# Optimization experiments

Measured on AMD Instinct MI355X. Metric: run time of the kernel, lower is better.

The kernel has to match this reference:

```python
import jax, jax.numpy as jnp
import numpy as np

NUM_HEADS = 16
EMB = 1024
HEAD = 64
SEQ = 2048
BATCH = 4


def setup_inputs() -> dict:
    key = jax.random.key(0)
    ks = jax.random.split(key, 6)
    s = EMB ** -0.5
    x = jax.random.normal(ks[0], (BATCH, SEQ, EMB), dtype=jnp.float32)
    # per-head projection weights stacked: [H, E, D] (Linear(emb, head, bias=False) per head)
    Wq = jax.random.normal(ks[1], (NUM_HEADS, EMB, HEAD), dtype=jnp.float32) * s
    Wk = jax.random.normal(ks[2], (NUM_HEADS, EMB, HEAD), dtype=jnp.float32) * s
    Wv = jax.random.normal(ks[3], (NUM_HEADS, EMB, HEAD), dtype=jnp.float32) * s
    # output projection Linear(head*num_heads, emb): weight [E, H*D], bias [E]
    Wo = jax.random.normal(ks[4], (EMB, NUM_HEADS * HEAD), dtype=jnp.float32) * ((NUM_HEADS * HEAD) ** -0.5)
    bo = jax.random.normal(ks[5], (EMB,), dtype=jnp.float32) * 0.01
    return {"x": x, "Wq": Wq, "Wk": Wk, "Wv": Wv, "Wo": Wo, "bo": bo}


def reference(x, Wq, Wk, Wv, Wo, bo):
    B, S, E = x.shape
    scale = HEAD ** -0.5
    # batched per-head projections: [B, H, S, D]
    q = jnp.einsum('bse,hed->bhsd', x, Wq)
    k = jnp.einsum('bse,hed->bhsd', x, Wk)
    v = jnp.einsum('bse,hed->bhsd', x, Wv)
    scores = jnp.einsum('bhqd,bhkd->bhqk', q, k) * scale
    causal = jnp.tril(jnp.ones((S, S), dtype=bool))
    scores = jnp.where(causal, scores, jnp.finfo(scores.dtype).min)
    attn = jax.nn.softmax(scores, axis=-1)  # dropout disabled (eval/deterministic)
    ctx = jnp.einsum('bhqk,bhkd->bhqd', attn, v)
    # concat heads along last dim (head-major order, matching torch.cat)
    concat = ctx.transpose(0, 2, 1, 3).reshape(B, S, NUM_HEADS * HEAD)
    out = concat @ Wo.T + bo
    return out
```

## Files before the change

kernel.cpp:

```cpp
#include <hip/hip_runtime.h>

#define NHEADS 16
#define EMB 1024
#define HDIM 64
#define SEQ 2048
#define BATCH 4

typedef unsigned short u16;
typedef __attribute__((ext_vector_type(8))) __bf16 bf16x8;
typedef __attribute__((ext_vector_type(4))) float f32x4;

#if __has_builtin(__builtin_amdgcn_exp2f)
#define EXP2(x) __builtin_amdgcn_exp2f(x)
#else
#define EXP2(x) __expf((x)*0.69314718056f)
#endif
#define CL2E 0.18033688011112042f

#define BARRIER() __builtin_amdgcn_s_barrier()
#define SB0() __builtin_amdgcn_sched_barrier(0)
#define PRIO1() __builtin_amdgcn_s_setprio(1)
#define PRIO0() __builtin_amdgcn_s_setprio(0)
#define VMCNT(n) asm volatile("s_waitcnt vmcnt(" #n ")" ::: "memory")
#define LGKM0() asm volatile("s_waitcnt lgkmcnt(0)" ::: "memory")

__device__ __forceinline__ u16 f2bf(float f) {
  union { float f; unsigned u; } v; v.f = f;
  unsigned r = v.u + 0x7fffu + ((v.u >> 16) & 1u);
  return (u16)(r >> 16);
}
__device__ __forceinline__ unsigned pk2bf(float a, float b) {
  union { __bf16 h[2]; unsigned u; } x;
  x.h[0] = (__bf16)a; x.h[1] = (__bf16)b; return x.u;
}
__device__ __forceinline__ void gl16(const void* g, void* l) {
  __builtin_amdgcn_global_load_lds(
      (const __attribute__((address_space(1))) unsigned*)g,
      (__attribute__((address_space(3))) unsigned*)l, 16, 0, 0);
}
__device__ __forceinline__ unsigned PKLO(unsigned a, unsigned b) {
  return __builtin_amdgcn_perm(a, b, 0x01000504u);
}
__device__ __forceinline__ unsigned PKHI(unsigned a, unsigned b) {
  return __builtin_amdgcn_perm(a, b, 0x03020706u);
}

__global__ __launch_bounds__(256) void k_prep(const float* __restrict__ x,
                                              const float* __restrict__ Wo,
                                              const float* __restrict__ Wq,
                                              const float* __restrict__ Wk,
                                              const float* __restrict__ Wv,
                                              u16* __restrict__ Xb,
                                              u16* __restrict__ Wob,
                                              u16* __restrict__ Wt) {
  __shared__ u16 sT[64][65];
  const int bid = blockIdx.x;
  const int t = threadIdx.x;
  if (bid < 8192) {
    int i = bid * 256 + t;
    f32x4 v = *(const f32x4*)(x + (size_t)i * 4);
    uint2 o;
    o.x = (unsigned)f2bf(v[0]) | ((unsigned)f2bf(v[1]) << 16);
    o.y = (unsigned)f2bf(v[2]) | ((unsigned)f2bf(v[3]) << 16);
    *(uint2*)(Xb + (size_t)i * 4) = o;
  } else if (bid < 9216) {
    int i = (bid - 8192) * 256 + t;
    f32x4 v = *(const f32x4*)(Wo + (size_t)i * 4);
    uint2 o;
    o.x = (unsigned)f2bf(v[0]) | ((unsigned)f2bf(v[1]) << 16);
    o.y = (unsigned)f2bf(v[2]) | ((unsigned)f2bf(v[3]) << 16);
    *(uint2*)(Wob + (size_t)i * 4) = o;
  } else {
    int pb = bid - 9216;
    const int mh = pb % 48;
    const int e0 = (pb / 48) * 64;
    const int mtx = mh >> 4, h = mh & 15;
    const float* W = (mtx == 0 ? Wq : (mtx == 1 ? Wk : Wv)) + (size_t)h * EMB * HDIM;
    {
      int e = t >> 2, d0 = (t & 3) * 16;
#pragma unroll
      for (int jj = 0; jj < 4; jj++) {
        f32x4 v = *(const f32x4*)(W + (size_t)(e0 + e) * HDIM + d0 + jj * 4);
#pragma unroll
        for (int kk = 0; kk < 4; kk++) sT[e][d0 + jj * 4 + kk] = f2bf(v[kk]);
      }
    }
    __syncthreads();
    {
      int d = t >> 2, eb = (t & 3) * 16;
#pragma unroll
      for (int j = 0; j < 16; j++)
        Wt[(size_t)(mh * 64 + d) * EMB + e0 + eb + j] = sT[eb + j][d];
    }
  }
}

__global__ __launch_bounds__(256) void k_gemm_qkv(const u16* __restrict__ Xb,
                                                  const u16* __restrict__ Wt,
                                                  u16* __restrict__ Q,
                                                  u16* __restrict__ K,
                                                  u16* __restrict__ V) {
  const int bid = blockIdx.x;
  const int l = (bid & 7) * 192 + (bid >> 3);
  const int mt = l % 64, nt = l / 64;
  const int m0 = mt * 128, n0 = nt * 128;
  const int t = threadIdx.x;
  const int wave = t >> 6, lane = t & 63, lr = lane & 15, lg = lane >> 4;
  const int wr = (wave >> 1) * 64, wc = (wave & 1) * 64;

  __shared__ __align__(16) char sA[128 * 128];
  __shared__ __align__(16) char sB[128 * 128];

  const f32x4 fz = {0.f, 0.f, 0.f, 0.f};
  f32x4 acc[4][4];
#pragma unroll
  for (int i = 0; i < 4; i++)
#pragma unroll
    for (int j = 0; j < 4; j++) acc[i][j] = fz;

  for (int k0 = 0; k0 < EMB; k0 += 64) {
#pragma unroll
    for (int i = 0; i < 4; i++) {
      int rb = wave * 32 + i * 8;
      int row = rb + (lane >> 3);
      int gc = (lane & 7) ^ (row & 7);
      gl16(Xb + (size_t)(m0 + row) * EMB + k0 + gc * 8, sA + rb * 128);
      gl16(Wt + (size_t)(n0 + row) * EMB + k0 + gc * 8, sB + rb * 128);
    }
    __syncthreads();
    bf16x8 af[4][2], bfr[4][2];
#pragma unroll
    for (int mf = 0; mf < 4; mf++)
#pragma unroll
      for (int kf = 0; kf < 2; kf++) {
        int row = wr + mf * 16 + lr;
        af[mf][kf] = *(const bf16x8*)(sA + row * 128 + ((kf * 64 + lg * 16) ^ ((row & 7) << 4)));
      }
#pragma unroll
    for (int nf = 0; nf < 4; nf++)
#pragma unroll
      for (int kf = 0; kf < 2; kf++) {
        int row = wc + nf * 16 + lr;
        bfr[nf][kf] = *(const bf16x8*)(sB + row * 128 + ((kf * 64 + lg * 16) ^ ((row & 7) << 4)));
      }
#pragma unroll
    for (int kf = 0; kf < 2; kf++)
#pragma unroll
      for (int mf = 0; mf < 4; mf++)
#pragma unroll
        for (int nf = 0; nf < 4; nf++)
          acc[mf][nf] = __builtin_amdgcn_mfma_f32_16x16x32_bf16(af[mf][kf], bfr[nf][kf], acc[mf][nf], 0, 0, 0);
    __syncthreads();
  }

  const int b = m0 >> 11;
  const int s0 = m0 & 2047;
#pragma unroll
  for (int mf = 0; mf < 4; mf++)
#pragma unroll
    for (int nf = 0; nf < 4; nf++)
#pragma unroll
      for (int r = 0; r < 4; r++) {
        int row = wr + mf * 16 + lg * 4 + r;
        int n = n0 + wc + nf * 16 + lr;
        int mtx = n >> 10, h = (n >> 6) & 15, d = n & 63;
        u16* dst = (mtx == 0 ? Q : (mtx == 1 ? K : V));
        dst[((size_t)(b * NHEADS + h) * SEQ + s0 + row) * HDIM + d] = f2bf(acc[mf][nf][r]);
      }
}

__global__ __launch_bounds__(256, 3) void k_attn(const u16* __restrict__ Q,
                                                 const u16* __restrict__ K,
                                                 const u16* __restrict__ V,
                                                 u16* __restrict__ Cc) {
  const int bh = blockIdx.x;
  const int qt = 15 - (int)blockIdx.y;
  const int b = bh >> 4, h = bh & 15;
  const int t = threadIdx.x;
  const int wq = t >> 6, lane = t & 63, lr = lane & 15, lg = lane >> 4;
  const size_t base = (size_t)bh * SEQ * HDIM;

  __shared__ __align__(16) char sK[2][64 * 128];
  __shared__ __align__(16) char sV[2][64 * 128];
  __shared__ __align__(16) char sP[128 * 128];

  const int kvb = (t & 15) * 4, db = (t >> 4) * 4;
  uint2 v0, v1, v2, v3;
  auto VLOAD = [&](int k0) {
    const u16* vp = V + base + (size_t)(k0 + kvb) * HDIM + db;
    v0 = *(const uint2*)(vp);
    v1 = *(const uint2*)(vp + HDIM);
    v2 = *(const uint2*)(vp + 2 * HDIM);
    v3 = *(const uint2*)(vp + 3 * HDIM);
  };
  auto VWRITE = [&](char* sv) {
    uint2 w0 = {PKLO(v0.x, v1.x), PKLO(v2.x, v3.x)};
    uint2 w1 = {PKHI(v0.x, v1.x), PKHI(v2.x, v3.x)};
    uint2 w2 = {PKLO(v0.y, v1.y), PKLO(v2.y, v3.y)};
    uint2 w3 = {PKHI(v0.y, v1.y), PKHI(v2.y, v3.y)};
    *(uint2*)(sv + (db + 0) * 128 + ((kvb * 2) ^ (((db + 0) & 7) << 4))) = w0;
    *(uint2*)(sv + (db + 1) * 128 + ((kvb * 2) ^ (((db + 1) & 7) << 4))) = w1;
    *(uint2*)(sv + (db + 2) * 128 + ((kvb * 2) ^ (((db + 2) & 7) << 4))) = w2;
    *(uint2*)(sv + (db + 3) * 128 + ((kvb * 2) ^ (((db + 3) & 7) << 4))) = w3;
  };
  auto KSTAGE = [&](char* sk, int k0) {
#pragma unroll
    for (int i = 0; i < 2; i++) {
      int rb = wq * 16 + i * 8;
      int row = rb + (lane >> 3);
      int gc = (lane & 7) ^ (row & 7);
      gl16(K + base + (size_t)(k0 + row) * HDIM + gc * 8, sk + rb * 128);
    }
  };

#pragma unroll
  for (int i = 0; i < 4; i++) {
    int rb = wq * 32 + i * 8;
    int row = rb + (lane >> 3);
    int gc = (lane & 7) ^ (row & 7);
    gl16(Q + base + (size_t)(qt * 128 + row) * HDIM + gc * 8, sP + rb * 128);
  }
  KSTAGE(sK[0], 0);
  VLOAD(0);
  VMCNT(0);
  VWRITE(sV[0]);
  __syncthreads();

  bf16x8 qf[2][2];
#pragma unroll
  for (int q2 = 0; q2 < 2; q2++)
#pragma unroll
    for (int kf = 0; kf < 2; kf++) {
      int row = wq * 32 + q2 * 16 + lr;
      qf[q2][kf] = *(const bf16x8*)(sP + row * 128 + ((kf * 64 + lg * 16) ^ ((row & 7) << 4)));
    }

  const f32x4 fz = {0.f, 0.f, 0.f, 0.f};
  f32x4 ot[4][2];
#pragma unroll
  for (int df = 0; df < 4; df++)
#pragma unroll
    for (int q2 = 0; q2 < 2; q2++) ot[df][q2] = fz;
  float l_[2] = {0.f, 0.f};
  const float nmc = -64.f * CL2E;

  const int nsteps = 2 * qt + 2;
  for (int step = 0; step < nsteps; step++) {
    const int k0 = step * 64;
    const int cur = step & 1, nxt = cur ^ 1;
    const bool pf = (step + 1 < nsteps);
    if (pf) {
      KSTAGE(sK[nxt], k0 + 64);
      VLOAD(k0 + 64);
    }

    f32x4 st[4][2];
#pragma unroll
    for (int kvf = 0; kvf < 4; kvf++)
#pragma unroll
      for (int q2 = 0; q2 < 2; q2++) st[kvf][q2] = fz;
#pragma unroll
    for (int kf = 0; kf < 2; kf++) {
      bf16x8 kfr[4];
#pragma unroll
      for (int kvf = 0; kvf < 4; kvf++) {
        int row = kvf * 16 + lr;
        kfr[kvf] = *(const bf16x8*)(sK[cur] + row * 128 + ((kf * 64 + lg * 16) ^ ((row & 7) << 4)));
      }
      PRIO1();
#pragma unroll
      for (int kvf = 0; kvf < 4; kvf++)
#pragma unroll
        for (int q2 = 0; q2 < 2; q2++)
          st[kvf][q2] = __builtin_amdgcn_mfma_f32_16x16x32_bf16(kfr[kvf], qf[q2][kf], st[kvf][q2], 0, 0, 0);
      PRIO0();
    }

    const bool diag = (k0 >= qt * 128);
#pragma unroll
    for (int q2 = 0; q2 < 2; q2++) {
      if (diag) {
        const int qg = qt * 128 + wq * 32 + q2 * 16 + lr;
#pragma unroll
        for (int kvf = 0; kvf < 4; kvf++)
#pragma unroll
          for (int r = 0; r < 4; r++)
            if (k0 + kvf * 16 + 4 * lg + r > qg) st[kvf][q2][r] = -3e38f;
      }
      const int prow = wq * 32 + q2 * 16 + lr;
      float rs = 0.f;
#pragma unroll
      for (int kvf = 0; kvf < 4; kvf++) {
        float p0 = EXP2(fmaf(st[kvf][q2][0], CL2E, nmc));
        float p1 = EXP2(fmaf(st[kvf][q2][1], CL2E, nmc));
        float p2 = EXP2(fmaf(st[kvf][q2][2], CL2E, nmc));
        float p3 = EXP2(fmaf(st[kvf][q2][3], CL2E, nmc));
        rs += (p0 + p1) + (p2 + p3);
        uint2 w;
        w.x = pk2bf(p0, p1);
        w.y = pk2bf(p2, p3);
        *(uint2*)(sP + prow * 128 + ((kvf * 32 + lg * 8) ^ ((prow & 7) << 4))) = w;
      }
      l_[q2] += rs;
    }

#pragma unroll
    for (int kf = 0; kf < 2; kf++) {
      bf16x8 pfg[2], vf[4];
#pragma unroll
      for (int q2 = 0; q2 < 2; q2++) {
        int row = wq * 32 + q2 * 16 + lr;
        pfg[q2] = *(const bf16x8*)(sP + row * 128 + ((kf * 64 + lg * 16) ^ ((row & 7) << 4)));
      }
#pragma unroll
      for (int df = 0; df < 4; df++) {
        int row = df * 16 + lr;
        vf[df] = *(const bf16x8*)(sV[cur] + row * 128 + ((kf * 64 + lg * 16) ^ ((row & 7) << 4)));
      }
      PRIO1();
#pragma unroll
      for (int df = 0; df < 4; df++)
#pragma unroll
        for (int q2 = 0; q2 < 2; q2++)
          ot[df][q2] = __builtin_amdgcn_mfma_f32_16x16x32_bf16(vf[df], pfg[q2], ot[df][q2], 0, 0, 0);
      PRIO0();
    }

    if (pf) {
      VMCNT(0);
      VWRITE(sV[nxt]);
      LGKM0();
      BARRIER();
    }
  }

#pragma unroll
  for (int q2 = 0; q2 < 2; q2++) {
    float l = l_[q2];
    l += __shfl_xor(l, 16);
    l += __shfl_xor(l, 32);
    float inv = 1.0f / l;
    int s = qt * 128 + wq * 32 + q2 * 16 + lr;
#pragma unroll
    for (int df = 0; df < 4; df++) {
      uint2 w;
      w.x = pk2bf(ot[df][q2][0] * inv, ot[df][q2][1] * inv);
      w.y = pk2bf(ot[df][q2][2] * inv, ot[df][q2][3] * inv);
      *(uint2*)(Cc + ((size_t)b * SEQ + s) * (NHEADS * HDIM) + h * HDIM + df * 16 + 4 * lg) = w;
    }
  }
}

__global__ __launch_bounds__(512, 2) void k_gemm_out8(const u16* __restrict__ Cc,
                                                      const u16* __restrict__ Wob,
                                                      const float* __restrict__ bo,
                                                      float* __restrict__ out) {
  extern __shared__ __align__(16) char smem[];
  const int bid = blockIdx.x;
  const int l = (bid & 7) * 32 + (bid >> 3);
  const int mt = l & 31, nt = l >> 5;
  const int m0 = mt * 256, n0 = nt * 128;

  const int t = threadIdx.x;
  const int wave = t >> 6, lane = t & 63, lr = lane & 15, lg = lane >> 4;
  const int wr = (wave >> 2) * 128;
  const int wc = (wave & 3) * 32;

  const f32x4 fz = {0.f, 0.f, 0.f, 0.f};
  f32x4 acc[8][2];
#pragma unroll
  for (int i = 0; i < 8; i++)
#pragma unroll
    for (int j = 0; j < 2; j++) acc[i][j] = fz;

  bf16x8 af[4][2], bfr[2][2];

  auto SROUND = [&](char* ldsbase, int rbase, const u16* src, int gRowBase, int kt) {
    int rs = rbase + wave * 8;
    int row = rs + (lane >> 3);
    int gc = (lane & 7) ^ (row & 7);
    gl16(src + (size_t)(gRowBase + row) * EMB + kt * 64 + gc * 8, ldsbase + rs * 128);
  };
  auto STAGE6 = [&](char* nA, char* nB, int kt) {
    SROUND(nB, 0, Wob, n0, kt); SROUND(nB, 64, Wob, n0, kt);
    SROUND(nA, 0, Cc, m0, kt); SROUND(nA, 64, Cc, m0, kt);
    SROUND(nA, 128, Cc, m0, kt); SROUND(nA, 192, Cc, m0, kt);
  };
  auto LOADA = [&](const char* bA, int mh) {
#pragma unroll
    for (int mf = 0; mf < 4; mf++)
#pragma unroll
      for (int kf = 0; kf < 2; kf++) {
        int row = wr + mh * 64 + mf * 16 + lr;
        af[mf][kf] = *(const bf16x8*)(bA + row * 128 + ((kf * 64 + lg * 16) ^ ((row & 7) << 4)));
      }
  };
  auto LOADB = [&](const char* bB) {
#pragma unroll
    for (int nf = 0; nf < 2; nf++)
#pragma unroll
      for (int kf = 0; kf < 2; kf++) {
        int row = wc + nf * 16 + lr;
        bfr[nf][kf] = *(const bf16x8*)(bB + row * 128 + ((kf * 64 + lg * 16) ^ ((row & 7) << 4)));
      }
  };

#define MFMAPH2(MH)                                                                        \
  do {                                                                                     \
    _Pragma("unroll") for (int kf = 0; kf < 2; kf++)                                       \
    _Pragma("unroll") for (int mf = 0; mf < 4; mf++)                                       \
    _Pragma("unroll") for (int nf = 0; nf < 2; nf++)                                       \
      acc[(MH)*4 + mf][nf] = __builtin_amdgcn_mfma_f32_16x16x32_bf16(                      \
          af[mf][kf], bfr[nf][kf], acc[(MH)*4 + mf][nf], 0, 0, 0);                         \
  } while (0)

  const int NT = EMB / 64;
  STAGE6(smem, smem + 32768, 0);
  VMCNT(0);
  BARRIER();

  for (int tt = 0; tt < NT - 1; tt++) {
    const int cb = tt & 1, nb = cb ^ 1;
    char* bA = smem + cb * 49152;
    char* bB = bA + 32768;
    char* nA = smem + nb * 49152;
    char* nB = nA + 32768;
    STAGE6(nA, nB, tt + 1);
    VMCNT(6);
    BARRIER(); SB0();
    LOADA(bA, 0);
    LOADB(bB);
    PRIO1(); MFMAPH2(0); PRIO0();
    LOADA(bA, 1);
    PRIO1(); MFMAPH2(1); PRIO0();
    BARRIER();
  }
  {
    char* bA = smem + ((NT - 1) & 1) * 49152;
    char* bB = bA + 32768;
    VMCNT(0);
    BARRIER(); SB0();
    LOADA(bA, 0);
    LOADB(bB);
    PRIO1(); MFMAPH2(0); PRIO0();
    LOADA(bA, 1);
    PRIO1(); MFMAPH2(1); PRIO0();
  }
#undef MFMAPH2

  float bv[2];
#pragma unroll
  for (int nf = 0; nf < 2; nf++) bv[nf] = bo[n0 + wc + nf * 16 + lr];
#pragma unroll
  for (int am = 0; am < 8; am++)
#pragma unroll
    for (int nf = 0; nf < 2; nf++)
#pragma unroll
      for (int r = 0; r < 4; r++) {
        int row = wr + am * 16 + lg * 4 + r;
        int n = n0 + wc + nf * 16 + lr;
        out[(size_t)(m0 + row) * EMB + n] = acc[am][nf][r] + bv[nf];
      }
}

extern "C" void kernel_launch(void* const* d_in, const int* in_sizes, int n_in,
                              void* d_out, int out_size, void* d_ws, size_t ws_size,
                              hipStream_t stream) {
  const float* x  = (const float*)d_in[0];
  const float* Wq = (const float*)d_in[1];
  const float* Wk = (const float*)d_in[2];
  const float* Wv = (const float*)d_in[3];
  const float* Wo = (const float*)d_in[4];
  const float* bo = (const float*)d_in[5];
  float* out = (float*)d_out;

  char* ws = (char*)d_ws;
  const size_t SZ_XB  = (size_t)8192 * 1024 * 2;
  const size_t SZ_WT  = (size_t)3072 * 1024 * 2;
  const size_t SZ_WOB = (size_t)1024 * 1024 * 2;
  const size_t SZ_QKV = (size_t)64 * 2048 * 64 * 2;
  u16* Xb  = (u16*)(ws);
  u16* Wt  = (u16*)(ws + SZ_XB);
  u16* Wob = (u16*)(ws + SZ_XB + SZ_WT);
  u16* Qb  = (u16*)(ws + SZ_XB + SZ_WT + SZ_WOB);
  u16* Kb  = (u16*)(ws + SZ_XB + SZ_WT + SZ_WOB + SZ_QKV);
  u16* Vb  = (u16*)(ws + SZ_XB + SZ_WT + SZ_WOB + 2 * SZ_QKV);
  u16* Cc  = (u16*)(ws + SZ_XB + SZ_WT + SZ_WOB + 3 * SZ_QKV);

  k_prep<<<9984, 256, 0, stream>>>(x, Wo, Wq, Wk, Wv, Xb, Wob, Wt);
  k_gemm_qkv<<<1536, 256, 0, stream>>>(Xb, Wt, Qb, Kb, Vb);
  k_attn<<<dim3(64, 16), 256, 0, stream>>>(Qb, Kb, Vb, Cc);
  k_gemm_out8<<<256, 512, 98304, stream>>>(Cc, Wob, bo, out);
}
```

Baseline: 171.7 us.

## Rewrite QKV GEMM as 256x128 triple-buffered pipeline and triple-buffer output GEMM

Result: no change. 169.9 us (-1.1%).

```diff
diff --git a/kernel.cpp b/kernel.cpp
--- a/kernel.cpp
+++ b/kernel.cpp
@@ -95,77 +95,103 @@
   }
 }
 
-__global__ __launch_bounds__(256) void k_gemm_qkv(const u16* __restrict__ Xb,
+__global__ __launch_bounds__(512) void k_gemm_qkv(const u16* __restrict__ Xb,
                                                   const u16* __restrict__ Wt,
                                                   u16* __restrict__ Q,
                                                   u16* __restrict__ K,
                                                   u16* __restrict__ V) {
+  extern __shared__ __align__(16) char smem[];
   const int bid = blockIdx.x;
-  const int l = (bid & 7) * 192 + (bid >> 3);
-  const int mt = l % 64, nt = l / 64;
-  const int m0 = mt * 128, n0 = nt * 128;
+  const int l = (bid & 7) * 96 + (bid >> 3);
+  const int mt = l % 32, nt = l / 32;
+  const int m0 = mt * 256, n0 = nt * 128;
+
   const int t = threadIdx.x;
   const int wave = t >> 6, lane = t & 63, lr = lane & 15, lg = lane >> 4;
-  const int wr = (wave >> 1) * 64, wc = (wave & 1) * 64;
-
-  __shared__ __align__(16) char sA[128 * 128];
-  __shared__ __align__(16) char sB[128 * 128];
+  const int wr = (wave >> 2) * 128;
+  const int wc = (wave & 3) * 32;
 
   const f32x4 fz = {0.f, 0.f, 0.f, 0.f};
-  f32x4 acc[4][4];
-#pragma unroll
-  for (int i = 0; i < 4; i++)
-#pragma unroll
-    for (int j = 0; j < 4; j++) acc[i][j] = fz;
-
-  for (int k0 = 0; k0 < EMB; k0 += 64) {
-#pragma unroll
-    for (int i = 0; i < 4; i++) {
-      int rb = wave * 32 + i * 8;
-      int row = rb + (lane >> 3);
-      int gc = (lane & 7) ^ (row & 7);
-      gl16(Xb + (size_t)(m0 + row) * EMB + k0 + gc * 8, sA + rb * 128);
-      gl16(Wt + (size_t)(n0 + row) * EMB + k0 + gc * 8, sB + rb * 128);
-    }
-    __syncthreads();
-    bf16x8 af[4][2], bfr[4][2];
+  f32x4 acc[8][2];
+#pragma unroll
+  for (int i = 0; i < 8; i++)
+#pragma unroll
+    for (int j = 0; j < 2; j++) acc[i][j] = fz;
+
+  bf16x8 af[4][2], bfr[2][2];
+
+  auto SROUND = [&](char* ldsbase, int rbase, const u16* src, int gRowBase, int kt) {
+    int rs = rbase + wave * 8;
+    int row = rs + (lane >> 3);
+    int gc = (lane & 7) ^ (row & 7);
+    gl16(src + (size_t)(gRowBase + row) * EMB + kt * 64 + gc * 8, ldsbase + rs * 128);
+  };
+  auto STAGE6 = [&](char* buf, int kt) {
+    SROUND(buf, 0, Xb, m0, kt); SROUND(buf, 64, Xb, m0, kt);
+    SROUND(buf, 128, Xb, m0, kt); SROUND(buf, 192, Xb, m0, kt);
+    SROUND(buf + 32768, 0, Wt, n0, kt); SROUND(buf + 32768, 64, Wt, n0, kt);
+  };
+  auto LOADA = [&](const char* bA, int mh) {
 #pragma unroll
     for (int mf = 0; mf < 4; mf++)
 #pragma unroll
       for (int kf = 0; kf < 2; kf++) {
-        int row = wr + mf * 16 + lr;
-        af[mf][kf] = *(const bf16x8*)(sA + row * 128 + ((kf * 64 + lg * 16) ^ ((row & 7) << 4)));
-      }
-#pragma unroll
-    for (int nf = 0; nf < 4; nf++)
+        int row = wr + mh * 64 + mf * 16 + lr;
+        af[mf][kf] = *(const bf16x8*)(bA + row * 128 + ((kf * 64 + lg * 16) ^ ((row & 7) << 4)));
+      }
+  };
+  auto LOADB = [&](const char* bB) {
+#pragma unroll
+    for (int nf = 0; nf < 2; nf++)
 #pragma unroll
       for (int kf = 0; kf < 2; kf++) {
         int row = wc + nf * 16 + lr;
-        bfr[nf][kf] = *(const bf16x8*)(sB + row * 128 + ((kf * 64 + lg * 16) ^ ((row & 7) << 4)));
-      }
-#pragma unroll
-    for (int kf = 0; kf < 2; kf++)
-#pragma unroll
-      for (int mf = 0; mf < 4; mf++)
-#pragma unroll
-        for (int nf = 0; nf < 4; nf++)
-          acc[mf][nf] = __builtin_amdgcn_mfma_f32_16x16x32_bf16(af[mf][kf], bfr[nf][kf], acc[mf][nf], 0, 0, 0);
-    __syncthreads();
+        bfr[nf][kf] = *(const bf16x8*)(bB + row * 128 + ((kf * 64 + lg * 16) ^ ((row & 7) << 4)));
+      }
+  };
+
+#define MFMAH(MH)                                                                          \
+  do {                                                                                     \
+    PRIO1();                                                                               \
+    _Pragma("unroll") for (int kf = 0; kf < 2; kf++)                                       \
+    _Pragma("unroll") for (int mf = 0; mf < 4; mf++)                                       \
+    _Pragma("unroll") for (int nf = 0; nf < 2; nf++)                                       \
+      acc[(MH)*4 + mf][nf] = __builtin_amdgcn_mfma_f32_16x16x32_bf16(                      \
+          af[mf][kf], bfr[nf][kf], acc[(MH)*4 + mf][nf], 0, 0, 0);                         \
+    PRIO0();                                                                               \
+  } while (0)
+
+  const int NT = EMB / 64;
+  STAGE6(smem, 0);
+  STAGE6(smem + 49152, 1);
+
+  for (int tt = 0; tt < NT; tt++) {
+    if (tt == NT - 1) { VMCNT(0); } else { VMCNT(6); }
+    BARRIER();
+    if (tt + 2 < NT) STAGE6(smem + ((tt + 2) % 3) * 49152, tt + 2);
+    char* bA = smem + (tt % 3) * 49152;
+    char* bB = bA + 32768;
+    LOADA(bA, 0);
+    LOADB(bB);
+    MFMAH(0);
+    LOADA(bA, 1);
+    MFMAH(1);
   }
+#undef MFMAH
 
   const int b = m0 >> 11;
   const int s0 = m0 & 2047;
 #pragma unroll
-  for (int mf = 0; mf < 4; mf++)
-#pragma unroll
-    for (int nf = 0; nf < 4; nf++)
+  for (int am = 0; am < 8; am++)
+#pragma unroll
+    for (int nf = 0; nf < 2; nf++)
 #pragma unroll
       for (int r = 0; r < 4; r++) {
-        int row = wr + mf * 16 + lg * 4 + r;
+        int row = wr + am * 16 + lg * 4 + r;
         int n = n0 + wc + nf * 16 + lr;
         int mtx = n >> 10, h = (n >> 6) & 15, d = n & 63;
         u16* dst = (mtx == 0 ? Q : (mtx == 1 ? K : V));
-        dst[((size_t)(b * NHEADS + h) * SEQ + s0 + row) * HDIM + d] = f2bf(acc[mf][nf][r]);
+        dst[((size_t)(b * NHEADS + h) * SEQ + s0 + row) * HDIM + d] = f2bf(acc[am][nf][r]);
       }
 }
 
@@ -351,14 +377,14 @@
   }
 }
 
-__global__ __launch_bounds__(512, 2) void k_gemm_out8(const u16* __restrict__ Cc,
-                                                      const u16* __restrict__ Wob,
-                                                      const float* __restrict__ bo,
-                                                      float* __restrict__ out) {
+__global__ __launch_bounds__(512) void k_gemm_out(const u16* __restrict__ Cc,
+                                                  const u16* __restrict__ Wob,
+                                                  const float* __restrict__ bo,
+                                                  float* __restrict__ out) {
   extern __shared__ __align__(16) char smem[];
   const int bid = blockIdx.x;
   const int l = (bid & 7) * 32 + (bid >> 3);
-  const int mt = l & 31, nt = l >> 5;
+  const int mt = l % 32, nt = l / 32;
   const int m0 = mt * 256, n0 = nt * 128;
 
   const int t = threadIdx.x;
@@ -381,10 +407,10 @@
     int gc = (lane & 7) ^ (row & 7);
     gl16(src + (size_t)(gRowBase + row) * EMB + kt * 64 + gc * 8, ldsbase + rs * 128);
   };
-  auto STAGE6 = [&](char* nA, char* nB, int kt) {
-    SROUND(nB, 0, Wob, n0, kt); SROUND(nB, 64, Wob, n0, kt);
-    SROUND(nA, 0, Cc, m0, kt); SROUND(nA, 64, Cc, m0, kt);
-    SROUND(nA, 128, Cc, m0, kt); SROUND(nA, 192, Cc, m0, kt);
+  auto STAGE6 = [&](char* buf, int kt) {
+    SROUND(buf, 0, Cc, m0, kt); SROUND(buf, 64, Cc, m0, kt);
+    SROUND(buf, 128, Cc, m0, kt); SROUND(buf, 192, Cc, m0, kt);
+    SROUND(buf + 32768, 0, Wob, n0, kt); SROUND(buf + 32768, 64, Wob, n0, kt);
   };
   auto LOADA = [&](const char* bA, int mh) {
 #pragma unroll
@@ -405,48 +431,34 @@
       }
   };
 
-#define MFMAPH2(MH)                                                                        \
+#define MFMAH2(MH)                                                                         \
   do {                                                                                     \
+    PRIO1();                                                                               \
     _Pragma("unroll") for (int kf = 0; kf < 2; kf++)                                       \
     _Pragma("unroll") for (int mf = 0; mf < 4; mf++)                                       \
     _Pragma("unroll") for (int nf = 0; nf < 2; nf++)                                       \
       acc[(MH)*4 + mf][nf] = __builtin_amdgcn_mfma_f32_16x16x32_bf16(                      \
           af[mf][kf], bfr[nf][kf], acc[(MH)*4 + mf][nf], 0, 0, 0);                         \
+    PRIO0();                                                                               \
   } while (0)
 
   const int NT = EMB / 64;
-  STAGE6(smem, smem + 32768, 0);
-  VMCNT(0);
-  BARRIER();
-
-  for (int tt = 0; tt < NT - 1; tt++) {
-    const int cb = tt & 1, nb = cb ^ 1;
-    char* bA = smem + cb * 49152;
+  STAGE6(smem, 0);
+  STAGE6(smem + 49152, 1);
+
+  for (int tt = 0; tt < NT; tt++) {
+    if (tt == NT - 1) { VMCNT(0); } else { VMCNT(6); }
+    BARRIER();
+    if (tt + 2 < NT) STAGE6(smem + ((tt + 2) % 3) * 49152, tt + 2);
+    char* bA = smem + (tt % 3) * 49152;
     char* bB = bA + 32768;
-    char* nA = smem + nb * 49152;
-    char* nB = nA + 32768;
-    STAGE6(nA, nB, tt + 1);
-    VMCNT(6);
-    BARRIER(); SB0();
     LOADA(bA, 0);
     LOADB(bB);
-    PRIO1(); MFMAPH2(0); PRIO0();
+    MFMAH2(0);
     LOADA(bA, 1);
-    PRIO1(); MFMAPH2(1); PRIO0();
-    BARRIER();
+    MFMAH2(1);
   }
-  {
-    char* bA = smem + ((NT - 1) & 1) * 49152;
-    char* bB = bA + 32768;
-    VMCNT(0);
-    BARRIER(); SB0();
-    LOADA(bA, 0);
-    LOADB(bB);
-    PRIO1(); MFMAPH2(0); PRIO0();
-    LOADA(bA, 1);
-    PRIO1(); MFMAPH2(1); PRIO0();
-  }
-#undef MFMAPH2
+#undef MFMAH2
 
   float bv[2];
 #pragma unroll
@@ -488,7 +500,7 @@
   u16* Cc  = (u16*)(ws + SZ_XB + SZ_WT + SZ_WOB + 3 * SZ_QKV);
 
   k_prep<<<9984, 256, 0, stream>>>(x, Wo, Wq, Wk, Wv, Xb, Wob, Wt);
-  k_gemm_qkv<<<1536, 256, 0, stream>>>(Xb, Wt, Qb, Kb, Vb);
+  k_gemm_qkv<<<768, 512, 147456, stream>>>(Xb, Wt, Qb, Kb, Vb);
   k_attn<<<dim3(64, 16), 256, 0, stream>>>(Qb, Kb, Vb, Cc);
-  k_gemm_out8<<<256, 512, 98304, stream>>>(Cc, Wob, bo, out);
-}
+  k_gemm_out<<<256, 512, 147456, stream>>>(Cc, Wob, bo, out);
+}
```
